# Optimization experiments

Measured on AMD Instinct MI355X. Metric: run time of the kernel, lower is better.

Reference implementation:

```python
import jax, jax.numpy as jnp
import numpy as np

E = 1024   # embed_dim
H = 16     # head_size
DH = E // H  # head_dim = 64
B, S = 2, 2048
SCALE = 1.0 / np.sqrt(E)  # original divides by sqrt(query.size(-1)) == sqrt(embed_dim)


def setup_inputs() -> dict:
    key = jax.random.key(0)
    ks = jax.random.split(key, 11)
    init = 0.02
    return {
        "query": jax.random.normal(ks[0], (B, S, E), dtype=jnp.float32),
        "key":   jax.random.normal(ks[1], (B, S, E), dtype=jnp.float32),
        "value": jax.random.normal(ks[2], (B, S, E), dtype=jnp.float32),
        # per-head projection weights, stacked over heads: [H, E, DH]
        "Wq": jax.random.normal(ks[3], (H, E, DH), dtype=jnp.float32) * init,
        "bq": jax.random.normal(ks[4], (H, DH), dtype=jnp.float32) * init,
        "Wk": jax.random.normal(ks[5], (H, E, DH), dtype=jnp.float32) * init,
        "bk": jax.random.normal(ks[6], (H, DH), dtype=jnp.float32) * init,
        "Wv": jax.random.normal(ks[7], (H, E, DH), dtype=jnp.float32) * init,
        "bv": jax.random.normal(ks[8], (H, DH), dtype=jnp.float32) * init,
        "Wo": jax.random.normal(ks[9], (E, E), dtype=jnp.float32) * init,
        "bo": jax.random.normal(ks[10], (E,), dtype=jnp.float32) * init,
    }


def reference(query, key, value, Wq, bq, Wk, bk, Wv, bv, Wo, bo):
    # per-head linear projections (vectorized over heads)
    q = jnp.einsum('bse,hed->bhsd', query, Wq) + bq[None, :, None, :]
    k = jnp.einsum('bse,hed->bhsd', key,   Wk) + bk[None, :, None, :]
    v = jnp.einsum('bse,hed->bhsd', value, Wv) + bv[None, :, None, :]
    # NOTE: original code scales by sqrt(embed_dim), not sqrt(head_dim)
    scores = jnp.einsum('bhqd,bhkd->bhqk', q, k) * SCALE
    weights = jax.nn.softmax(scores, axis=-1)
    out = jnp.einsum('bhqk,bhkd->bhqd', weights, v)  # [B,H,S,DH]
    # concat heads along last dim (head order == stacking order)
    out = out.transpose(0, 2, 1, 3).reshape(B, S, H * DH)
    return out @ Wo + bo
```

## Files before the change

### kernel.cpp

```cpp
#include <hip/hip_runtime.h>

typedef __bf16 bf16;
typedef __bf16 bf16x8 __attribute__((ext_vector_type(8)));
typedef __bf16 bf16x4 __attribute__((ext_vector_type(4)));
typedef __bf16 bf16x2 __attribute__((ext_vector_type(2)));
typedef float f32x4 __attribute__((ext_vector_type(4)));
typedef float f32x16 __attribute__((ext_vector_type(16)));

#define MM 4096
#define NN 1024
#define KK 1024

__device__ __forceinline__ void gload_lds16(const void* g, void* l) {
  __builtin_amdgcn_global_load_lds(
      (const __attribute__((address_space(1))) void*)g,
      (__attribute__((address_space(3))) void*)l, 16, 0, 0);
}

__global__ __launch_bounds__(256) void cvt_all(const float* __restrict__ q,
                                               const float* __restrict__ k,
                                               const float* __restrict__ v,
                                               const float* __restrict__ Wq,
                                               const float* __restrict__ Wk,
                                               const float* __restrict__ Wv,
                                               const float* __restrict__ Wo,
                                               bf16* __restrict__ Xb,
                                               bf16* __restrict__ Wt,
                                               bf16* __restrict__ Wot)
{
  __shared__ bf16 Sl[64 * 72];
  const int bid = blockIdx.x;
  const int t = threadIdx.x;

  if (bid < 12288) {
    int p = bid >> 12, bx = bid & 4095;
    const float* src = (p == 0) ? q : (p == 1 ? k : v);
    bf16* dst = Xb + (size_t)p * (MM * (size_t)KK);
    int i = (bx * 256 + t) * 4;
    float4 val = *(const float4*)(src + i);
    bf16x4 o;
    o.x = (bf16)val.x; o.y = (bf16)val.y; o.z = (bf16)val.z; o.w = (bf16)val.w;
    *(bf16x4*)(dst + i) = o;
    return;
  }

  const int wb = bid - 12288;
  const int p = wb >> 8, t8 = wb & 255;
  const int ti = t >> 4, c4 = (t & 15) * 4;

  if (p < 3) {
    const float* W = (p == 0) ? Wq : (p == 1 ? Wk : Wv);
    const int h = t8 >> 4, e0 = (t8 & 15) << 6;
#pragma unroll
    for (int r = 0; r < 4; ++r) {
      int e_l = r * 16 + ti;
      float4 val = *(const float4*)(W + (h << 16) + (e0 + e_l) * 64 + c4);
      bf16x4 o; o.x = (bf16)val.x; o.y = (bf16)val.y; o.z = (bf16)val.z; o.w = (bf16)val.w;
      *(bf16x4*)(Sl + e_l * 72 + c4) = o;
    }
    __syncthreads();
#pragma unroll
    for (int r = 0; r < 4; ++r) {
      int d_l = r * 16 + ti;
      bf16x4 o;
      o.x = Sl[(c4 + 0) * 72 + d_l];
      o.y = Sl[(c4 + 1) * 72 + d_l];
      o.z = Sl[(c4 + 2) * 72 + d_l];
      o.w = Sl[(c4 + 3) * 72 + d_l];
      *(bf16x4*)(Wt + (size_t)p * 1048576 + (size_t)((h << 6) + d_l) * 1024 + e0 + c4) = o;
    }
  } else {
    const int n0 = (t8 >> 4) << 6, k0 = (t8 & 15) << 6;
#pragma unroll
    for (int r = 0; r < 4; ++r) {
      int k_l = r * 16 + ti;
      float4 val = *(const float4*)(Wo + (size_t)(k0 + k_l) * 1024 + n0 + c4);
      bf16x4 o; o.x = (bf16)val.x; o.y = (bf16)val.y; o.z = (bf16)val.z; o.w = (bf16)val.w;
      *(bf16x4*)(Sl + k_l * 72 + c4) = o;
    }
    __syncthreads();
#pragma unroll
    for (int r = 0; r < 4; ++r) {
      int n_l = r * 16 + ti;
      bf16x4 o;
      o.x = Sl[(c4 + 0) * 72 + n_l];
      o.y = Sl[(c4 + 1) * 72 + n_l];
      o.z = Sl[(c4 + 2) * 72 + n_l];
      o.w = Sl[(c4 + 3) * 72 + n_l];
      *(bf16x4*)(Wot + (size_t)(n0 + n_l) * 1024 + k0 + c4) = o;
    }
  }
}

__device__ __forceinline__ void gemm_body(const bf16* __restrict__ A,
                                          const bf16* __restrict__ Bt,
                                          bf16* As, bf16* Bs,
                                          int m0, int n0, f32x4 (&acc)[4][4])
{
  const int tid = threadIdx.x;
  const int w = tid >> 6, L = tid & 63;
  const int quad = L >> 4, l16 = L & 15;
  const int wm = (w & 1) << 6, wn = (w >> 1) << 6;

  const bf16* Ag = A + (size_t)(m0 + w * 32 + (L >> 2)) * KK + (L & 3) * 8;
  const bf16* Bg = Bt + (size_t)(n0 + w * 32 + (L >> 2)) * KK + (L & 3) * 8;
  bf16* Al = As + w * 1024;
  bf16* Bl = Bs + w * 1024;

  for (int kt = 0; kt < KK / 32; ++kt) {
    __syncthreads();
    const bf16* a0 = Ag + kt * 32;
    const bf16* b0 = Bg + kt * 32;
    gload_lds16(a0, Al);
    gload_lds16(a0 + 16 * KK, Al + 512);
    gload_lds16(b0, Bl);
    gload_lds16(b0 + 16 * KK, Bl + 512);
    __syncthreads();
    bf16x8 af[4], bfr[4];
#pragma unroll
    for (int mi = 0; mi < 4; ++mi)
      af[mi] = *(const bf16x8*)(As + (wm + mi * 16 + l16) * 32 + quad * 8);
#pragma unroll
    for (int ni = 0; ni < 4; ++ni)
      bfr[ni] = *(const bf16x8*)(Bs + (wn + ni * 16 + l16) * 32 + quad * 8);
#pragma unroll
    for (int mi = 0; mi < 4; ++mi)
#pragma unroll
      for (int ni = 0; ni < 4; ++ni)
        acc[mi][ni] = __builtin_amdgcn_mfma_f32_16x16x32_bf16(af[mi], bfr[ni],
                                                              acc[mi][ni], 0, 0, 0);
  }
}

__global__ __launch_bounds__(256) void gemm_proj(const bf16* __restrict__ X,
                                                 const bf16* __restrict__ Wt,
                                                 const float* __restrict__ b0,
                                                 const float* __restrict__ b1,
                                                 const float* __restrict__ b2,
                                                 bf16* __restrict__ Out)
{
  __shared__ bf16 As[4096], Bs[4096];
  int p = blockIdx.y;
  const bf16* A = X + (size_t)p * 4194304;
  const bf16* Bt = Wt + (size_t)p * 1048576;
  const float* bias = (p == 0) ? b0 : (p == 1 ? b1 : b2);
  bf16* C = Out + (size_t)p * 4194304;
  int bx = blockIdx.x;
  int m0 = (bx >> 3) << 7, n0 = (bx & 7) << 7;
  f32x4 acc[4][4] = {};
  gemm_body(A, Bt, As, Bs, m0, n0, acc);
  const int L = threadIdx.x & 63, w = threadIdx.x >> 6;
  const int quad = L >> 4, l16 = L & 15;
  const int wm = (w & 1) << 6, wn = (w >> 1) << 6;
#pragma unroll
  for (int ni = 0; ni < 4; ++ni) {
    int col = n0 + wn + ni * 16 + l16;
    float bv = bias[col];
#pragma unroll
    for (int mi = 0; mi < 4; ++mi)
#pragma unroll
      for (int r = 0; r < 4; ++r) {
        int row = m0 + wm + mi * 16 + quad * 4 + r;
        C[(size_t)row * NN + col] = (bf16)(acc[mi][ni][r] + bv);
      }
  }
}

__global__ __launch_bounds__(256) void gemm_outp(const bf16* __restrict__ A,
                                                 const bf16* __restrict__ Bt,
                                                 const float* __restrict__ bias,
                                                 float* __restrict__ C)
{
  __shared__ bf16 As[2048], Bs[4096];
  const int bx = blockIdx.x;
  const int m0 = (bx >> 3) << 6, n0 = (bx & 7) << 7;
  const int tid = threadIdx.x;
  const int w = tid >> 6, L = tid & 63;
  const int quad = L >> 4, l16 = L & 15;
  const int wm = (w & 1) << 5, wn = (w >> 1) << 6;

  const bf16* Ag = A + (size_t)(m0 + w * 16 + (L >> 2)) * KK + (L & 3) * 8;
  const bf16* Bg = Bt + (size_t)(n0 + w * 32 + (L >> 2)) * KK + (L & 3) * 8;
  bf16* Al = As + w * 512;
  bf16* Bl = Bs + w * 1024;

  f32x4 acc[2][4] = {};
  for (int kt = 0; kt < KK / 32; ++kt) {
    __syncthreads();
    const bf16* a0 = Ag + kt * 32;
    const bf16* b0 = Bg + kt * 32;
    gload_lds16(a0, Al);
    gload_lds16(b0, Bl);
    gload_lds16(b0 + 16 * KK, Bl + 512);
    __syncthreads();
    bf16x8 af[2], bfr[4];
#pragma unroll
    for (int mi = 0; mi < 2; ++mi)
      af[mi] = *(const bf16x8*)(As + (wm + mi * 16 + l16) * 32 + quad * 8);
#pragma unroll
    for (int ni = 0; ni < 4; ++ni)
      bfr[ni] = *(const bf16x8*)(Bs + (wn + ni * 16 + l16) * 32 + quad * 8);
#pragma unroll
    for (int mi = 0; mi < 2; ++mi)
#pragma unroll
      for (int ni = 0; ni < 4; ++ni)
        acc[mi][ni] = __builtin_amdgcn_mfma_f32_16x16x32_bf16(af[mi], bfr[ni],
                                                              acc[mi][ni], 0, 0, 0);
  }

#pragma unroll
  for (int ni = 0; ni < 4; ++ni) {
    int col = n0 + wn + ni * 16 + l16;
    float bv = bias[col];
#pragma unroll
    for (int mi = 0; mi < 2; ++mi)
#pragma unroll
      for (int r = 0; r < 4; ++r) {
        int row = m0 + wm + mi * 16 + quad * 4 + r;
        C[(size_t)row * NN + col] = acc[mi][ni][r] + bv;
      }
  }
}

__global__ __launch_bounds__(256) void flash_attn(const bf16* __restrict__ Qm,
                                                  const bf16* __restrict__ Km,
                                                  const bf16* __restrict__ Vm,
                                                  bf16* __restrict__ Om)
{
  __shared__ bf16 Kl[64 * 64];
  __shared__ bf16 Vt[64 * 64];
  __shared__ bf16 Pl[4][32 * 64];

  const int tid = threadIdx.x;
  const int w = tid >> 6, L = tid & 63;
  const int l32 = L & 31, hi = L >> 5;
  const int bh = blockIdx.x & 31;
  const int qb = blockIdx.x >> 5;
  const int b = bh >> 4, h = bh & 15;
  const int s0 = qb << 7;
  const size_t base = (size_t)b * 2097152 + h * 64;

  bf16x8 qf[4];
  const float SL = 0.03125f * 1.44269504088896f;
  {
    const bf16* qp = Qm + base + (size_t)(s0 + w * 32 + l32) * 1024 + hi * 8;
#pragma unroll
    for (int s = 0; s < 4; ++s) {
      bf16x8 tq = *(const bf16x8*)(qp + s * 16);
#pragma unroll
      for (int j = 0; j < 8; ++j) tq[j] = (bf16)((float)tq[j] * SL);
      qf[s] = tq;
    }
  }

  bf16x8 onesf;
#pragma unroll
  for (int j = 0; j < 8; ++j) onesf[j] = (bf16)1.0f;

  f32x16 oacc0 = {}, oacc1 = {}, lacc = {};

  const bf16* Kg = Km + base + (size_t)(2 * l32 + hi) * 1024 + w * 16;
  const int dh8 = w * 16 + hi * 8;
  const bf16* Vg = Vm + base + (size_t)(2 * l32) * 1024 + dh8;
  bf16* Pw = &Pl[w][0];
  const int r7 = l32 & 7;

  bf16x8 k0 = *(const bf16x8*)Kg;
  bf16x8 k1 = *(const bf16x8*)(Kg + 8);
  bf16x8 va = *(const bf16x8*)Vg;
  bf16x8 vb = *(const bf16x8*)(Vg + 1024);

  for (int kt = 0; kt < 32; ++kt) {
    __syncthreads();
    *(bf16x8*)(Kl + L * 64 + ((((2 * w + 0) ^ (L & 7)) << 3))) = k0;
    *(bf16x8*)(Kl + L * 64 + ((((2 * w + 1) ^ (L & 7)) << 3))) = k1;
#pragma unroll
    for (int j = 0; j < 8; ++j) {
      int row = dh8 + j;
      bf16x2 pr; pr.x = va[j]; pr.y = vb[j];
      *(bf16x2*)(Vt + row * 64 + (((l32 >> 2) ^ (row & 7)) << 3) + ((l32 & 3) << 1)) = pr;
    }
    if (kt + 1 < 32) {
      k0 = *(const bf16x8*)(Kg + (size_t)(kt + 1) * 65536);
      k1 = *(const bf16x8*)(Kg + (size_t)(kt + 1) * 65536 + 8);
      va = *(const bf16x8*)(Vg + (size_t)(kt + 1) * 65536);
      vb = *(const bf16x8*)(Vg + (size_t)(kt + 1) * 65536 + 1024);
    }
    __syncthreads();

    f32x16 sa = {}, sb = {};
#pragma unroll
    for (int s = 0; s < 4; ++s) {
      bf16x8 kfa = *(const bf16x8*)(Kl + (l32)      * 64 + (((2 * s + hi) ^ r7) << 3));
      bf16x8 kfb = *(const bf16x8*)(Kl + (32 + l32) * 64 + (((2 * s + hi) ^ r7) << 3));
      sa = __builtin_amdgcn_mfma_f32_32x32x16_bf16(qf[s], kfa, sa, 0, 0, 0);
      sb = __builtin_amdgcn_mfma_f32_32x32x16_bf16(qf[s], kfb, sb, 0, 0, 0);
    }

#pragma unroll
    for (int reg = 0; reg < 16; ++reg) {
      int row = (reg & 3) + ((reg >> 2) << 3) + (hi << 2);
      float p0 = __builtin_amdgcn_exp2f(sa[reg]);
      float p1 = __builtin_amdgcn_exp2f(sb[reg]);
      bf16x2 pv; pv.x = (bf16)p0; pv.y = (bf16)p1;
      *(bf16x2*)(Pw + row * 64 + (((l32 >> 2) ^ (row & 7)) << 3) + ((l32 & 3) << 1)) = pv;
    }
    asm volatile("s_waitcnt lgkmcnt(0)" ::: "memory");

#pragma unroll
    for (int s = 0; s < 4; ++s) {
      bf16x8 paf = *(const bf16x8*)(Pw + l32 * 64 + (((2 * s + hi) ^ r7) << 3));
      bf16x8 vf0 = *(const bf16x8*)(Vt + (l32)      * 64 + (((2 * s + hi) ^ r7) << 3));
      bf16x8 vf1 = *(const bf16x8*)(Vt + (32 + l32) * 64 + (((2 * s + hi) ^ r7) << 3));
      oacc0 = __builtin_amdgcn_mfma_f32_32x32x16_bf16(paf, vf0, oacc0, 0, 0, 0);
      oacc1 = __builtin_amdgcn_mfma_f32_32x32x16_bf16(paf, vf1, oacc1, 0, 0, 0);
      lacc  = __builtin_amdgcn_mfma_f32_32x32x16_bf16(paf, onesf, lacc, 0, 0, 0);
    }
  }

#pragma unroll
  for (int reg = 0; reg < 16; ++reg) {
    int row = (reg & 3) + ((reg >> 2) << 3) + (hi << 2);
    float inv = 1.f / lacc[reg];
    bf16* op = Om + base + (size_t)(s0 + w * 32 + row) * 1024;
    op[l32]      = (bf16)(oacc0[reg] * inv);
    op[32 + l32] = (bf16)(oacc1[reg] * inv);
  }
}

extern "C" void kernel_launch(void* const* d_in, const int* in_sizes, int n_in,
                              void* d_out, int out_size, void* d_ws, size_t ws_size,
                              hipStream_t stream)
{
  const float* q  = (const float*)d_in[0];
  const float* k  = (const float*)d_in[1];
  const float* v  = (const float*)d_in[2];
  const float* Wq = (const float*)d_in[3];
  const float* bq = (const float*)d_in[4];
  const float* Wk = (const float*)d_in[5];
  const float* bk = (const float*)d_in[6];
  const float* Wv = (const float*)d_in[7];
  const float* bv = (const float*)d_in[8];
  const float* Wo = (const float*)d_in[9];
  const float* bo = (const float*)d_in[10];

  char* ws = (char*)d_ws;
  bf16* Xb  = (bf16*)ws;
  bf16* Wt  = (bf16*)(ws + 25165824);
  bf16* Wot = (bf16*)(ws + 31457280);
  bf16* QKV = (bf16*)(ws + 33554432);
  bf16* O   = (bf16*)ws;

  cvt_all<<<dim3(13312), 256, 0, stream>>>(q, k, v, Wq, Wk, Wv, Wo, Xb, Wt, Wot);
  gemm_proj<<<dim3(256, 3), 256, 0, stream>>>(Xb, Wt, bq, bk, bv, QKV);
  flash_attn<<<dim3(512), 256, 0, stream>>>(QKV, QKV + 4194304, QKV + 8388608, O);
  gemm_outp<<<dim3(512), 256, 0, stream>>>(O, Wot, bo, (float*)d_out);
}
```

Baseline: 229.7 us.

## Double-buffer flash-attention K/V tiles, sum softmax rows in registers, deepen GEMM k-step

The flash-attention kernel now double-buffers K and V in LDS, writing the next tile while the current one is consumed. This leaves one barrier per iteration instead of two. The row-sum MFMA against a ones vector is replaced by per-lane fp32 accumulation of the exponentials plus a cross-lane shuffle reduction at the end, which frees matrix-core issue slots. Both GEMM kernels load 64-wide K slices per barrier pair instead of 32, halving barrier count at the cost of doubled LDS use and lower possible occupancy.

```diff
diff --git a/kernel.cpp b/kernel.cpp
--- a/kernel.cpp
+++ b/kernel.cpp
@@ -92,10 +92,10 @@
   }
 }
 
-__device__ __forceinline__ void gemm_body(const bf16* __restrict__ A,
-                                          const bf16* __restrict__ Bt,
-                                          bf16* As, bf16* Bs,
-                                          int m0, int n0, f32x4 (&acc)[4][4])
+__device__ __forceinline__ void gemm_body64(const bf16* __restrict__ A,
+                                            const bf16* __restrict__ Bt,
+                                            bf16* As, bf16* Bs,
+                                            int m0, int n0, f32x4 (&acc)[4][4])
 {
   const int tid = threadIdx.x;
   const int w = tid >> 6, L = tid & 63;
@@ -107,28 +107,35 @@
   bf16* Al = As + w * 1024;
   bf16* Bl = Bs + w * 1024;
 
-  for (int kt = 0; kt < KK / 32; ++kt) {
-    __syncthreads();
-    const bf16* a0 = Ag + kt * 32;
-    const bf16* b0 = Bg + kt * 32;
+  for (int kt = 0; kt < KK / 64; ++kt) {
+    __syncthreads();
+    const bf16* a0 = Ag + kt * 64;
+    const bf16* b0 = Bg + kt * 64;
     gload_lds16(a0, Al);
     gload_lds16(a0 + 16 * KK, Al + 512);
+    gload_lds16(a0 + 32, Al + 4096);
+    gload_lds16(a0 + 16 * KK + 32, Al + 4096 + 512);
     gload_lds16(b0, Bl);
     gload_lds16(b0 + 16 * KK, Bl + 512);
-    __syncthreads();
-    bf16x8 af[4], bfr[4];
-#pragma unroll
-    for (int mi = 0; mi < 4; ++mi)
-      af[mi] = *(const bf16x8*)(As + (wm + mi * 16 + l16) * 32 + quad * 8);
-#pragma unroll
-    for (int ni = 0; ni < 4; ++ni)
-      bfr[ni] = *(const bf16x8*)(Bs + (wn + ni * 16 + l16) * 32 + quad * 8);
-#pragma unroll
-    for (int mi = 0; mi < 4; ++mi)
+    gload_lds16(b0 + 32, Bl + 4096);
+    gload_lds16(b0 + 16 * KK + 32, Bl + 4096 + 512);
+    __syncthreads();
+#pragma unroll
+    for (int ks = 0; ks < 2; ++ks) {
+      bf16x8 af[4], bfr[4];
+#pragma unroll
+      for (int mi = 0; mi < 4; ++mi)
+        af[mi] = *(const bf16x8*)(As + ks * 4096 + (wm + mi * 16 + l16) * 32 + quad * 8);
 #pragma unroll
       for (int ni = 0; ni < 4; ++ni)
-        acc[mi][ni] = __builtin_amdgcn_mfma_f32_16x16x32_bf16(af[mi], bfr[ni],
-                                                              acc[mi][ni], 0, 0, 0);
+        bfr[ni] = *(const bf16x8*)(Bs + ks * 4096 + (wn + ni * 16 + l16) * 32 + quad * 8);
+#pragma unroll
+      for (int mi = 0; mi < 4; ++mi)
+#pragma unroll
+        for (int ni = 0; ni < 4; ++ni)
+          acc[mi][ni] = __builtin_amdgcn_mfma_f32_16x16x32_bf16(af[mi], bfr[ni],
+                                                                acc[mi][ni], 0, 0, 0);
+    }
   }
 }
 
@@ -139,7 +146,7 @@
                                                  const float* __restrict__ b2,
                                                  bf16* __restrict__ Out)
 {
-  __shared__ bf16 As[4096], Bs[4096];
+  __shared__ bf16 As[8192], Bs[8192];
   int p = blockIdx.y;
   const bf16* A = X + (size_t)p * 4194304;
   const bf16* Bt = Wt + (size_t)p * 1048576;
@@ -148,7 +155,7 @@
   int bx = blockIdx.x;
   int m0 = (bx >> 3) << 7, n0 = (bx & 7) << 7;
   f32x4 acc[4][4] = {};
-  gemm_body(A, Bt, As, Bs, m0, n0, acc);
+  gemm_body64(A, Bt, As, Bs, m0, n0, acc);
   const int L = threadIdx.x & 63, w = threadIdx.x >> 6;
   const int quad = L >> 4, l16 = L & 15;
   const int wm = (w & 1) << 6, wn = (w >> 1) << 6;
@@ -171,7 +178,7 @@
                                                  const float* __restrict__ bias,
                                                  float* __restrict__ C)
 {
-  __shared__ bf16 As[2048], Bs[4096];
+  __shared__ bf16 As[4096], Bs[8192];
   const int bx = blockIdx.x;
   const int m0 = (bx >> 3) << 6, n0 = (bx & 7) << 7;
   const int tid = threadIdx.x;
@@ -185,27 +192,33 @@
   bf16* Bl = Bs + w * 1024;
 
   f32x4 acc[2][4] = {};
-  for (int kt = 0; kt < KK / 32; ++kt) {
-    __syncthreads();
-    const bf16* a0 = Ag + kt * 32;
-    const bf16* b0 = Bg + kt * 32;
+  for (int kt = 0; kt < KK / 64; ++kt) {
+    __syncthreads();
+    const bf16* a0 = Ag + kt * 64;
+    const bf16* b0 = Bg + kt * 64;
     gload_lds16(a0, Al);
+    gload_lds16(a0 + 32, Al + 2048);
     gload_lds16(b0, Bl);
     gload_lds16(b0 + 16 * KK, Bl + 512);
-    __syncthreads();
-    bf16x8 af[2], bfr[4];
-#pragma unroll
-    for (int mi = 0; mi < 2; ++mi)
-      af[mi] = *(const bf16x8*)(As + (wm + mi * 16 + l16) * 32 + quad * 8);
-#pragma unroll
-    for (int ni = 0; ni < 4; ++ni)
-      bfr[ni] = *(const bf16x8*)(Bs + (wn + ni * 16 + l16) * 32 + quad * 8);
-#pragma unroll
-    for (int mi = 0; mi < 2; ++mi)
+    gload_lds16(b0 + 32, Bl + 4096);
+    gload_lds16(b0 + 16 * KK + 32, Bl + 4096 + 512);
+    __syncthreads();
+#pragma unroll
+    for (int ks = 0; ks < 2; ++ks) {
+      bf16x8 af[2], bfr[4];
+#pragma unroll
+      for (int mi = 0; mi < 2; ++mi)
+        af[mi] = *(const bf16x8*)(As + ks * 2048 + (wm + mi * 16 + l16) * 32 + quad * 8);
 #pragma unroll
       for (int ni = 0; ni < 4; ++ni)
-        acc[mi][ni] = __builtin_amdgcn_mfma_f32_16x16x32_bf16(af[mi], bfr[ni],
-                                                              acc[mi][ni], 0, 0, 0);
+        bfr[ni] = *(const bf16x8*)(Bs + ks * 4096 + (wn + ni * 16 + l16) * 32 + quad * 8);
+#pragma unroll
+      for (int mi = 0; mi < 2; ++mi)
+#pragma unroll
+        for (int ni = 0; ni < 4; ++ni)
+          acc[mi][ni] = __builtin_amdgcn_mfma_f32_16x16x32_bf16(af[mi], bfr[ni],
+                                                                acc[mi][ni], 0, 0, 0);
+    }
   }
 
 #pragma unroll
@@ -227,9 +240,9 @@
                                                   const bf16* __restrict__ Vm,
                                                   bf16* __restrict__ Om)
 {
-  __shared__ bf16 Kl[64 * 64];
-  __shared__ bf16 Vt[64 * 64];
-  __shared__ bf16 Pl[4][32 * 64];
+  __shared__ bf16 Kl[2][4096];
+  __shared__ bf16 Vt[2][4096];
+  __shared__ bf16 Pl[4][2048];
 
   const int tid = threadIdx.x;
   const int w = tid >> 6, L = tid & 63;
@@ -253,11 +266,10 @@
     }
   }
 
-  bf16x8 onesf;
-#pragma unroll
-  for (int j = 0; j < 8; ++j) onesf[j] = (bf16)1.0f;
-
-  f32x16 oacc0 = {}, oacc1 = {}, lacc = {};
+  f32x16 oacc0 = {}, oacc1 = {};
+  float lp[16];
+#pragma unroll
+  for (int i = 0; i < 16; ++i) lp[i] = 0.f;
 
   const bf16* Kg = Km + base + (size_t)(2 * l32 + hi) * 1024 + w * 16;
   const int dh8 = w * 16 + hi * 8;
@@ -269,30 +281,53 @@
   bf16x8 k1 = *(const bf16x8*)(Kg + 8);
   bf16x8 va = *(const bf16x8*)Vg;
   bf16x8 vb = *(const bf16x8*)(Vg + 1024);
-
-  for (int kt = 0; kt < 32; ++kt) {
-    __syncthreads();
-    *(bf16x8*)(Kl + L * 64 + ((((2 * w + 0) ^ (L & 7)) << 3))) = k0;
-    *(bf16x8*)(Kl + L * 64 + ((((2 * w + 1) ^ (L & 7)) << 3))) = k1;
+  {
+    bf16* KlS = &Kl[0][0];
+    bf16* VtS = &Vt[0][0];
+    *(bf16x8*)(KlS + L * 64 + (((2 * w + 0) ^ (L & 7)) << 3)) = k0;
+    *(bf16x8*)(KlS + L * 64 + (((2 * w + 1) ^ (L & 7)) << 3)) = k1;
 #pragma unroll
     for (int j = 0; j < 8; ++j) {
       int row = dh8 + j;
       bf16x2 pr; pr.x = va[j]; pr.y = vb[j];
-      *(bf16x2*)(Vt + row * 64 + (((l32 >> 2) ^ (row & 7)) << 3) + ((l32 & 3) << 1)) = pr;
-    }
+      *(bf16x2*)(VtS + row * 64 + (((l32 >> 2) ^ (row & 7)) << 3) + ((l32 & 3) << 1)) = pr;
+    }
+  }
+  k0 = *(const bf16x8*)(Kg + 65536);
+  k1 = *(const bf16x8*)(Kg + 65536 + 8);
+  va = *(const bf16x8*)(Vg + 65536);
+  vb = *(const bf16x8*)(Vg + 65536 + 1024);
+  __syncthreads();
+
+  for (int kt = 0; kt < 32; ++kt) {
+    const int cur = kt & 1, nxt = cur ^ 1;
+    const bf16* Kc = &Kl[cur][0];
+    const bf16* Vc = &Vt[cur][0];
+
     if (kt + 1 < 32) {
-      k0 = *(const bf16x8*)(Kg + (size_t)(kt + 1) * 65536);
-      k1 = *(const bf16x8*)(Kg + (size_t)(kt + 1) * 65536 + 8);
-      va = *(const bf16x8*)(Vg + (size_t)(kt + 1) * 65536);
-      vb = *(const bf16x8*)(Vg + (size_t)(kt + 1) * 65536 + 1024);
-    }
-    __syncthreads();
+      bf16* KlS = &Kl[nxt][0];
+      bf16* VtS = &Vt[nxt][0];
+      *(bf16x8*)(KlS + L * 64 + (((2 * w + 0) ^ (L & 7)) << 3)) = k0;
+      *(bf16x8*)(KlS + L * 64 + (((2 * w + 1) ^ (L & 7)) << 3)) = k1;
+#pragma unroll
+      for (int j = 0; j < 8; ++j) {
+        int row = dh8 + j;
+        bf16x2 pr; pr.x = va[j]; pr.y = vb[j];
+        *(bf16x2*)(VtS + row * 64 + (((l32 >> 2) ^ (row & 7)) << 3) + ((l32 & 3) << 1)) = pr;
+      }
+    }
+    if (kt + 2 < 32) {
+      k0 = *(const bf16x8*)(Kg + (size_t)(kt + 2) * 65536);
+      k1 = *(const bf16x8*)(Kg + (size_t)(kt + 2) * 65536 + 8);
+      va = *(const bf16x8*)(Vg + (size_t)(kt + 2) * 65536);
+      vb = *(const bf16x8*)(Vg + (size_t)(kt + 2) * 65536 + 1024);
+    }
 
     f32x16 sa = {}, sb = {};
 #pragma unroll
     for (int s = 0; s < 4; ++s) {
-      bf16x8 kfa = *(const bf16x8*)(Kl + (l32)      * 64 + (((2 * s + hi) ^ r7) << 3));
-      bf16x8 kfb = *(const bf16x8*)(Kl + (32 + l32) * 64 + (((2 * s + hi) ^ r7) << 3));
+      bf16x8 kfa = *(const bf16x8*)(Kc + (l32)      * 64 + (((2 * s + hi) ^ r7) << 3));
+      bf16x8 kfb = *(const bf16x8*)(Kc + (32 + l32) * 64 + (((2 * s + hi) ^ r7) << 3));
       sa = __builtin_amdgcn_mfma_f32_32x32x16_bf16(qf[s], kfa, sa, 0, 0, 0);
       sb = __builtin_amdgcn_mfma_f32_32x32x16_bf16(qf[s], kfb, sb, 0, 0, 0);
     }
@@ -302,6 +337,7 @@
       int row = (reg & 3) + ((reg >> 2) << 3) + (hi << 2);
       float p0 = __builtin_amdgcn_exp2f(sa[reg]);
       float p1 = __builtin_amdgcn_exp2f(sb[reg]);
+      lp[reg] += p0 + p1;
       bf16x2 pv; pv.x = (bf16)p0; pv.y = (bf16)p1;
       *(bf16x2*)(Pw + row * 64 + (((l32 >> 2) ^ (row & 7)) << 3) + ((l32 & 3) << 1)) = pv;
     }
@@ -310,18 +346,24 @@
 #pragma unroll
     for (int s = 0; s < 4; ++s) {
       bf16x8 paf = *(const bf16x8*)(Pw + l32 * 64 + (((2 * s + hi) ^ r7) << 3));
-      bf16x8 vf0 = *(const bf16x8*)(Vt + (l32)      * 64 + (((2 * s + hi) ^ r7) << 3));
-      bf16x8 vf1 = *(const bf16x8*)(Vt + (32 + l32) * 64 + (((2 * s + hi) ^ r7) << 3));
+      bf16x8 vf0 = *(const bf16x8*)(Vc + (l32)      * 64 + (((2 * s + hi) ^ r7) << 3));
+      bf16x8 vf1 = *(const bf16x8*)(Vc + (32 + l32) * 64 + (((2 * s + hi) ^ r7) << 3));
       oacc0 = __builtin_amdgcn_mfma_f32_32x32x16_bf16(paf, vf0, oacc0, 0, 0, 0);
       oacc1 = __builtin_amdgcn_mfma_f32_32x32x16_bf16(paf, vf1, oacc1, 0, 0, 0);
-      lacc  = __builtin_amdgcn_mfma_f32_32x32x16_bf16(paf, onesf, lacc, 0, 0, 0);
-    }
+    }
+    __syncthreads();
   }
 
 #pragma unroll
   for (int reg = 0; reg < 16; ++reg) {
+    float l = lp[reg];
+    l += __shfl_xor(l, 1);
+    l += __shfl_xor(l, 2);
+    l += __shfl_xor(l, 4);
+    l += __shfl_xor(l, 8);
+    l += __shfl_xor(l, 16);
     int row = (reg & 3) + ((reg >> 2) << 3) + (hi << 2);
-    float inv = 1.f / lacc[reg];
+    float inv = 1.f / l;
     bf16* op = Om + base + (size_t)(s0 + w * 32 + row) * 1024;
     op[l32]      = (bf16)(oacc0[reg] * inv);
     op[32 + l32] = (bf16)(oacc1[reg] * inv);
```

After: 233.3 us. No clear change (+1.6%).

## Split attention over two KV halves with a separate combine kernel

Applied to the files above, without the earlier changes.

Each attention block now processes only half of the key/value sequence, doubling the grid to improve occupancy across compute units. The unnormalized partial outputs (bf16) and row sums are written to workspace, and a new combine kernel sums the two halves and normalizes. This adds an extra kernel launch and partial-result memory traffic, plus slight precision loss from storing partials in bf16.

```diff
diff --git a/kernel.cpp b/kernel.cpp
--- a/kernel.cpp
+++ b/kernel.cpp
@@ -225,7 +225,8 @@
 __global__ __launch_bounds__(256) void flash_attn(const bf16* __restrict__ Qm,
                                                   const bf16* __restrict__ Km,
                                                   const bf16* __restrict__ Vm,
-                                                  bf16* __restrict__ Om)
+                                                  bf16* __restrict__ PO,
+                                                  float* __restrict__ PL)
 {
   __shared__ bf16 Kl[64 * 64];
   __shared__ bf16 Vt[64 * 64];
@@ -234,11 +235,14 @@
   const int tid = threadIdx.x;
   const int w = tid >> 6, L = tid & 63;
   const int l32 = L & 31, hi = L >> 5;
-  const int bh = blockIdx.x & 31;
-  const int qb = blockIdx.x >> 5;
+  const int bid = blockIdx.x;
+  const int bh = bid & 31;
+  const int half = (bid >> 5) & 1;
+  const int qb = bid >> 6;
   const int b = bh >> 4, h = bh & 15;
   const int s0 = qb << 7;
   const size_t base = (size_t)b * 2097152 + h * 64;
+  const size_t koff = (size_t)half * 1048576;
 
   bf16x8 qf[4];
   const float SL = 0.03125f * 1.44269504088896f;
@@ -259,9 +263,9 @@
 
   f32x16 oacc0 = {}, oacc1 = {}, lacc = {};
 
-  const bf16* Kg = Km + base + (size_t)(2 * l32 + hi) * 1024 + w * 16;
+  const bf16* Kg = Km + base + koff + (size_t)(2 * l32 + hi) * 1024 + w * 16;
   const int dh8 = w * 16 + hi * 8;
-  const bf16* Vg = Vm + base + (size_t)(2 * l32) * 1024 + dh8;
+  const bf16* Vg = Vm + base + koff + (size_t)(2 * l32) * 1024 + dh8;
   bf16* Pw = &Pl[w][0];
   const int r7 = l32 & 7;
 
@@ -270,7 +274,7 @@
   bf16x8 va = *(const bf16x8*)Vg;
   bf16x8 vb = *(const bf16x8*)(Vg + 1024);
 
-  for (int kt = 0; kt < 32; ++kt) {
+  for (int kt = 0; kt < 16; ++kt) {
     __syncthreads();
     *(bf16x8*)(Kl + L * 64 + ((((2 * w + 0) ^ (L & 7)) << 3))) = k0;
     *(bf16x8*)(Kl + L * 64 + ((((2 * w + 1) ^ (L & 7)) << 3))) = k1;
@@ -280,7 +284,7 @@
       bf16x2 pr; pr.x = va[j]; pr.y = vb[j];
       *(bf16x2*)(Vt + row * 64 + (((l32 >> 2) ^ (row & 7)) << 3) + ((l32 & 3) << 1)) = pr;
     }
-    if (kt + 1 < 32) {
+    if (kt + 1 < 16) {
       k0 = *(const bf16x8*)(Kg + (size_t)(kt + 1) * 65536);
       k1 = *(const bf16x8*)(Kg + (size_t)(kt + 1) * 65536 + 8);
       va = *(const bf16x8*)(Vg + (size_t)(kt + 1) * 65536);
@@ -318,13 +322,46 @@
     }
   }
 
+  const size_t slot = (size_t)(half * 512 + bh * 16 + qb);
+  bf16* po = PO + slot * 8192;
+  float* pl = PL + slot * 128;
 #pragma unroll
   for (int reg = 0; reg < 16; ++reg) {
     int row = (reg & 3) + ((reg >> 2) << 3) + (hi << 2);
-    float inv = 1.f / lacc[reg];
-    bf16* op = Om + base + (size_t)(s0 + w * 32 + row) * 1024;
-    op[l32]      = (bf16)(oacc0[reg] * inv);
-    op[32 + l32] = (bf16)(oacc1[reg] * inv);
+    int rg = w * 32 + row;
+    po[rg * 64 + l32]      = (bf16)oacc0[reg];
+    po[rg * 64 + 32 + l32] = (bf16)oacc1[reg];
+    if (l32 == 0) pl[rg] = lacc[reg];
+  }
+}
+
+__global__ __launch_bounds__(256) void combine(const bf16* __restrict__ PO,
+                                               const float* __restrict__ PL,
+                                               bf16* __restrict__ Om)
+{
+  const int bid = blockIdx.x;
+  const int bh = bid & 31, qb = bid >> 5;
+  const int b = bh >> 4, h = bh & 15;
+  const int t = threadIdx.x;
+  const int q0 = t >> 3, d8 = (t & 7) * 8;
+  const size_t slot0 = (size_t)(bh * 16 + qb);
+  const bf16* po0 = PO + slot0 * 8192;
+  const bf16* po1 = PO + (slot0 + 512) * 8192;
+  const float* pl0 = PL + slot0 * 128;
+  const float* pl1 = PL + (slot0 + 512) * 128;
+  const size_t obase = (size_t)b * 2097152 + (size_t)(qb * 128) * 1024 + h * 64;
+
+#pragma unroll
+  for (int rep = 0; rep < 4; ++rep) {
+    int qq = rep * 32 + q0;
+    bf16x8 a = *(const bf16x8*)(po0 + qq * 64 + d8);
+    bf16x8 c = *(const bf16x8*)(po1 + qq * 64 + d8);
+    float inv = 1.f / (pl0[qq] + pl1[qq]);
+    bf16x8 o;
+#pragma unroll
+    for (int j = 0; j < 8; ++j)
+      o[j] = (bf16)(((float)a[j] + (float)c[j]) * inv);
+    *(bf16x8*)(Om + obase + (size_t)qq * 1024 + d8) = o;
   }
 }
 
@@ -345,14 +382,17 @@
   const float* bo = (const float*)d_in[10];
 
   char* ws = (char*)d_ws;
-  bf16* Xb  = (bf16*)ws;
-  bf16* Wt  = (bf16*)(ws + 25165824);
-  bf16* Wot = (bf16*)(ws + 31457280);
-  bf16* QKV = (bf16*)(ws + 33554432);
-  bf16* O   = (bf16*)ws;
+  bf16*  Xb  = (bf16*)ws;
+  bf16*  Wt  = (bf16*)(ws + 25165824);
+  bf16*  Wot = (bf16*)(ws + 31457280);
+  bf16*  QKV = (bf16*)(ws + 33554432);
+  bf16*  PO  = (bf16*)ws;
+  float* PL  = (float*)(ws + 16777216);
+  bf16*  O   = (bf16*)(ws + 18874368);
 
   cvt_all<<<dim3(13312), 256, 0, stream>>>(q, k, v, Wq, Wk, Wv, Wo, Xb, Wt, Wot);
   gemm_proj<<<dim3(256, 3), 256, 0, stream>>>(Xb, Wt, bq, bk, bv, QKV);
-  flash_attn<<<dim3(512), 256, 0, stream>>>(QKV, QKV + 4194304, QKV + 8388608, O);
+  flash_attn<<<dim3(1024), 256, 0, stream>>>(QKV, QKV + 4194304, QKV + 8388608, PO, PL);
+  combine<<<dim3(512), 256, 0, stream>>>(PO, PL, O);
   gemm_outp<<<dim3(512), 256, 0, stream>>>(O, Wot, bo, (float*)d_out);
 }
```

Result: no change. 233.9 us (+1.8%).
